# Performance work log

Measured on AMD Instinct MI355X. Metric: run time of the kernel, lower is better.

Reference implementation:

```python
import jax, jax.numpy as jnp
import numpy as np

N_NODES = 50000
N_EDGES = 800000
IN_CH = 256
HID = 64
HEADS = 4
NEG_SLOPE = 0.2  # PyG GATConv default


def setup_inputs() -> dict:
    key = jax.random.key(0)
    ks = jax.random.split(key, 12)
    glorot = lambda k, shape: jax.random.normal(k, shape, jnp.float32) * (2.0 / (shape[0] + shape[-1])) ** 0.5
    d1 = HEADS * HID  # 256: width after conv1 (concat heads)
    return {
        "x": jax.random.normal(ks[0], (N_NODES, IN_CH), jnp.float32),
        "edge_index": jax.random.randint(ks[1], (2, N_EDGES), 0, N_NODES, jnp.int64),
        # conv1: GATConv(IN_CH, HID, heads=HEADS)
        "W1": glorot(ks[2], (IN_CH, HEADS * HID)),
        "a_src1": glorot(ks[3], (HEADS, HID)),
        "a_dst1": glorot(ks[4], (HEADS, HID)),
        "b1": jnp.zeros((HEADS * HID,), jnp.float32),
        # conv2: GATConv(d1, d1, heads=1)
        "W2": glorot(ks[5], (d1, d1)),
        "a_src2": glorot(ks[6], (1, d1)),
        "a_dst2": glorot(ks[7], (1, d1)),
        "b2": jnp.zeros((d1,), jnp.float32),
    }


def gat_conv(x, src, dst, W, a_src, a_dst, b, heads, out_ch, n_nodes):
    """PyG-style GATConv: per-head linear, additive attention, segment softmax over dst."""
    h = (x @ W).reshape(n_nodes, heads, out_ch)            # [N, H, C]
    alpha_src = jnp.sum(h * a_src, axis=-1)                # [N, H]
    alpha_dst = jnp.sum(h * a_dst, axis=-1)                # [N, H]
    e = jax.nn.leaky_relu(alpha_src[src] + alpha_dst[dst], NEG_SLOPE)  # [E, H]
    # numerically-stable segment softmax grouped by destination node
    e_max = jax.ops.segment_max(e, dst, num_segments=n_nodes)         # [N, H]
    e_exp = jnp.exp(e - e_max[dst])
    denom = jax.ops.segment_sum(e_exp, dst, num_segments=n_nodes)
    alpha = e_exp / denom[dst]                                        # [E, H]
    out = jax.ops.segment_sum(alpha[:, :, None] * h[src], dst, num_segments=n_nodes)  # [N, H, C]
    return out.reshape(n_nodes, heads * out_ch) + b


def reference(x, edge_index, W1, a_src1, a_dst1, b1, W2, a_src2, a_dst2, b2):
    n = x.shape[0]
    loops = jnp.arange(n, dtype=edge_index.dtype)
    src = jnp.concatenate([edge_index[0], loops])  # add self-loops (PyG default)
    dst = jnp.concatenate([edge_index[1], loops])
    h1 = gat_conv(x, src, dst, W1, a_src1, a_dst1, b1, HEADS, HID, n)
    h1 = jax.nn.elu(h1)
    out = gat_conv(h1, src, dst, W2, a_src2, a_dst2, b2, 1, HEADS * HID, n)
    return out
```

## Files before the change

### kernel.cpp

```cpp
#include <hip/hip_runtime.h>
#include <stdint.h>

typedef __bf16 bfv8 __attribute__((ext_vector_type(8)));
typedef float f32x4 __attribute__((ext_vector_type(4)));

__device__ __forceinline__ float b2f(unsigned short u) {
    union { unsigned int i; float f; } v; v.i = ((unsigned int)u) << 16; return v.f;
}
__device__ __forceinline__ unsigned short f2b(float f) {
    unsigned int x = __float_as_uint(f);
    unsigned int r = x + 0x7FFFu + ((x >> 16) & 1u);
    return (unsigned short)(r >> 16);
}
__device__ __forceinline__ float squash(float v) {
    return (v == v && fabsf(v) < 1e30f) ? v : 0.f;
}
__device__ __forceinline__ float blo(unsigned int w) {
    union { unsigned int i; float f; } v; v.i = w << 16; return v.f;
}
__device__ __forceinline__ float bhi(unsigned int w) {
    union { unsigned int i; float f; } v; v.i = w & 0xffff0000u; return v.f;
}

__device__ __forceinline__ void detect_reg(const void* x, const void* ei, int& f32w, int& i64w) {
    const unsigned short* xu = (const unsigned short*)x;
    const int* e32 = (const int*)ei;
    int bad = 0, oz = 0;
#pragma unroll
    for (int j = 0; j < 64; j++) {
        float v = b2f(xu[j]);
        if (!(fabsf(v) < 1e10f)) bad++;
    }
#pragma unroll
    for (int j = 1; j < 16; j += 2)
        if (e32[j] == 0) oz++;
    f32w = (bad >= 2) ? 1 : 0;
    i64w = (oz >= 6) ? 1 : 0;
}

__device__ __forceinline__ int edge_at(const void* ei, int idx, int i64) {
    return i64 ? (int)(((const long long*)ei)[idx]) : ((const int*)ei)[idx];
}

__global__ __launch_bounds__(256) void k_prep(
        const void* __restrict__ x, const void* __restrict__ ei,
        const void* __restrict__ W1, const void* __restrict__ W2,
        const void* __restrict__ a_src1, const void* __restrict__ a_dst1, const void* __restrict__ b1,
        const void* __restrict__ a_src2, const void* __restrict__ a_dst2, const void* __restrict__ b2,
        unsigned short* __restrict__ xb, unsigned short* __restrict__ WT1,
        unsigned short* __restrict__ WT2, unsigned short* __restrict__ vecs,
        int* __restrict__ deg, int* __restrict__ flags,
        int E, int ET, int N, int total8, int nconv, int nhist) {
    __shared__ unsigned short t[32][33];
    int f32w, i64w;
    detect_reg(x, ei, f32w, i64w);
    int b = blockIdx.x;
    int tid = threadIdx.x;

    if (b < nconv) {
        int i = b * 256 + tid;
        if (i >= total8) return;
        if (f32w) {
            const float4* f = (const float4*)x;
            float4 a = f[2 * i], bb = f[2 * i + 1];
            uint4 o;
            o.x = (unsigned)f2b(squash(a.x)) | ((unsigned)f2b(squash(a.y)) << 16);
            o.y = (unsigned)f2b(squash(a.z)) | ((unsigned)f2b(squash(a.w)) << 16);
            o.z = (unsigned)f2b(squash(bb.x)) | ((unsigned)f2b(squash(bb.y)) << 16);
            o.w = (unsigned)f2b(squash(bb.z)) | ((unsigned)f2b(squash(bb.w)) << 16);
            *(uint4*)(xb + 8 * (size_t)i) = o;
        } else {
            *(uint4*)(xb + 8 * (size_t)i) = ((const uint4*)x)[i];
        }
    } else if (b < nconv + 128) {
        int tb2 = b - nconv;
        const void* W = (tb2 < 64) ? W1 : W2;
        unsigned short* WT = (tb2 < 64) ? WT1 : WT2;
        int t6 = tb2 & 63;
        int bx = (t6 & 7) * 32, by = (t6 >> 3) * 32;
        int tx = tid & 31, ty = tid >> 5;
        for (int j = 0; j < 32; j += 8) {
            size_t idx = (size_t)(by + ty + j) * 256 + bx + tx;
            t[ty + j][tx] = f32w ? f2b(squash(((const float*)W)[idx]))
                                 : ((const unsigned short*)W)[idx];
        }
        __syncthreads();
        for (int j = 0; j < 32; j += 8)
            WT[(size_t)(bx + ty + j) * 256 + by + tx] = t[tx][ty + j];
    } else if (b < nconv + 128 + nhist) {
        int i = (b - nconv - 128) * 256 + tid;
        if (i >= ET) return;
        int d = (i < E) ? edge_at(ei, E + i, i64w) : (i - E);
        d = min(max(d, 0), N - 1);
        atomicAdd(&deg[d], 1);
    } else {
        const void* ptrs[6] = {a_src1, a_dst1, b1, a_src2, a_dst2, b2};
#pragma unroll
        for (int j = 0; j < 6; j++) {
            unsigned short u = f32w ? f2b(squash(((const float*)ptrs[j])[tid]))
                                    : ((const unsigned short*)ptrs[j])[tid];
            vecs[j * 256 + tid] = u;
        }
        if (tid == 0) { flags[0] = f32w; flags[1] = i64w; }
    }
}

__global__ void k_scan1(const int* __restrict__ deg, int* __restrict__ tscan, int* __restrict__ bsum, int n) {
    __shared__ int sm[256];
    int tid = threadIdx.x;
    int i = blockIdx.x * 256 + tid;
    int v = (i < n) ? deg[i] : 0;
    sm[tid] = v; __syncthreads();
    for (int off = 1; off < 256; off <<= 1) {
        int t = (tid >= off) ? sm[tid - off] : 0;
        __syncthreads();
        sm[tid] += t;
        __syncthreads();
    }
    if (i < n) tscan[i] = sm[tid];
    if (tid == 255) bsum[blockIdx.x] = sm[255];
}

__global__ void k_scan2(const int* __restrict__ bsum, int* __restrict__ boff, int nb) {
    __shared__ int sm[256];
    int tid = threadIdx.x;
    int v = (tid < nb) ? bsum[tid] : 0;
    sm[tid] = v; __syncthreads();
    for (int off = 1; off < 256; off <<= 1) {
        int t = (tid >= off) ? sm[tid - off] : 0;
        __syncthreads();
        sm[tid] += t;
        __syncthreads();
    }
    if (tid < nb) boff[tid] = sm[tid] - v;
}

__global__ void k_scan3(const int* __restrict__ deg, const int* __restrict__ tscan,
                        const int* __restrict__ boff, int* __restrict__ row_start,
                        int* __restrict__ cursor, unsigned short* __restrict__ csr16,
                        int n, int ET) {
    int i = blockIdx.x * 256 + threadIdx.x;
    if (i < n) {
        int rs = tscan[i] - deg[i] + boff[i >> 8];
        row_start[i] = rs;
        cursor[i] = rs;
    }
    if (i == 0) row_start[n] = ET;
    if (blockIdx.x == 0 && threadIdx.x < 64) csr16[ET + threadIdx.x] = 0;
}

__global__ void k_scatter(const void* __restrict__ ei, int* __restrict__ cursor,
                          unsigned short* __restrict__ csr16, const int* __restrict__ flags,
                          int E, int ET, int N) {
    int i = blockIdx.x * 256 + threadIdx.x;
    if (i >= ET) return;
    int s, d;
    if (i < E) {
        int i64 = flags[1];
        s = edge_at(ei, i, i64);
        d = edge_at(ei, E + i, i64);
    } else {
        s = i - E; d = i - E;
    }
    s = min(max(s, 0), N - 1);
    d = min(max(d, 0), N - 1);
    int pos = atomicAdd(&cursor[d], 1);
    pos = min(max(pos, 0), ET - 1);
    csr16[pos] = (unsigned short)s;
}

__global__ __launch_bounds__(256) void k_gemm(const unsigned short* __restrict__ A,
                                              const unsigned short* __restrict__ BT,
                                              unsigned short* __restrict__ C, int M) {
    __shared__ __align__(16) unsigned short As[128 * 72];
    __shared__ __align__(16) unsigned short Bs[128 * 72];
    const int tid = threadIdx.x;
    const int m0 = blockIdx.x * 128, n0 = blockIdx.y * 128;
    const int w = tid >> 6, lane = tid & 63;
    const int wm = (w & 1) * 64, wn = (w >> 1) * 64;
    const int lr = lane & 15, lk = (lane >> 4) * 8;
    const int sr = tid >> 1, sc = (tid & 1) * 32;

    f32x4 acc[4][4];
#pragma unroll
    for (int a = 0; a < 4; a++)
#pragma unroll
        for (int b = 0; b < 4; b++) acc[a][b] = (f32x4){0.f, 0.f, 0.f, 0.f};

    for (int k0 = 0; k0 < 256; k0 += 64) {
        uint4 va0, va1, va2, va3;
        if (m0 + sr < M) {
            const uint4* Ap = (const uint4*)(A + (size_t)(m0 + sr) * 256 + k0 + sc);
            va0 = Ap[0]; va1 = Ap[1]; va2 = Ap[2]; va3 = Ap[3];
        } else {
            va0 = va1 = va2 = va3 = make_uint4(0, 0, 0, 0);
        }
        {
            uint4* Ad = (uint4*)&As[sr * 72 + sc];
            Ad[0] = va0; Ad[1] = va1; Ad[2] = va2; Ad[3] = va3;
        }
        {
            const uint4* Bp = (const uint4*)(BT + (size_t)(n0 + sr) * 256 + k0 + sc);
            uint4* Bd = (uint4*)&Bs[sr * 72 + sc];
            Bd[0] = Bp[0]; Bd[1] = Bp[1]; Bd[2] = Bp[2]; Bd[3] = Bp[3];
        }
        __syncthreads();
#pragma unroll
        for (int kk = 0; kk < 64; kk += 32) {
            bfv8 af[4], bfr[4];
#pragma unroll
            for (int mi = 0; mi < 4; mi++)
                af[mi] = *(const bfv8*)&As[(wm + mi * 16 + lr) * 72 + kk + lk];
#pragma unroll
            for (int ni = 0; ni < 4; ni++)
                bfr[ni] = *(const bfv8*)&Bs[(wn + ni * 16 + lr) * 72 + kk + lk];
#pragma unroll
            for (int mi = 0; mi < 4; mi++)
#pragma unroll
                for (int ni = 0; ni < 4; ni++)
                    acc[mi][ni] = __builtin_amdgcn_mfma_f32_16x16x32_bf16(af[mi], bfr[ni], acc[mi][ni], 0, 0, 0);
        }
        __syncthreads();
    }
    const int rb = (lane >> 4) * 4;
#pragma unroll
    for (int mi = 0; mi < 4; mi++) {
#pragma unroll
        for (int r = 0; r < 4; r++) {
            int row = m0 + wm + mi * 16 + rb + r;
            if (row < M) {
#pragma unroll
                for (int ni = 0; ni < 4; ni++)
                    C[(size_t)row * 256 + n0 + wn + ni * 16 + lr] = f2b(squash(acc[mi][ni][r]));
            }
        }
    }
}

__global__ void k_alphas(const unsigned short* __restrict__ Hm, const unsigned short* __restrict__ a_src,
                         const unsigned short* __restrict__ a_dst, float* __restrict__ as_out,
                         float* __restrict__ ad_out, int N, int H) {
    int wid = (blockIdx.x * 256 + threadIdx.x) >> 6;
    int lane = threadIdx.x & 63;
    if (wid >= N) return;
    int c = 4 * lane;
    uint2 hv = *(const uint2*)(Hm + (size_t)wid * 256 + c);
    float h0 = b2f((unsigned short)(hv.x & 0xffff));
    float h1 = b2f((unsigned short)(hv.x >> 16));
    float h2 = b2f((unsigned short)(hv.y & 0xffff));
    float h3 = b2f((unsigned short)(hv.y >> 16));
    float s = h0 * b2f(a_src[c]) + h1 * b2f(a_src[c + 1]) + h2 * b2f(a_src[c + 2]) + h3 * b2f(a_src[c + 3]);
    float d = h0 * b2f(a_dst[c]) + h1 * b2f(a_dst[c + 1]) + h2 * b2f(a_dst[c + 2]) + h3 * b2f(a_dst[c + 3]);
    int lph = 64 / H;
    for (int off = 1; off < lph; off <<= 1) {
        s += __shfl_xor(s, off, 64);
        d += __shfl_xor(d, off, 64);
    }
    if ((lane & (lph - 1)) == 0) {
        int h = lane / lph;
        as_out[(size_t)wid * H + h] = squash(s);
        ad_out[(size_t)wid * H + h] = squash(d);
    }
}

__global__ __launch_bounds__(256) void k_agg(
        const unsigned short* __restrict__ Hm, const float* __restrict__ asrc,
        const float* __restrict__ adst, const int* __restrict__ row_start,
        const unsigned short* __restrict__ csr16, const unsigned short* __restrict__ bias,
        void* __restrict__ out, const int* __restrict__ flags,
        int N, int H, int ET, int elu, int is_final) {
    __shared__ __align__(16) float lwv[8][32][4];
    __shared__ unsigned int loff[8][32];
    const int tid = threadIdx.x;
    const int hw = tid >> 5;
    const int l = tid & 31;
    const int node = blockIdx.x * 8 + hw;
    if (node >= N) return;
    const int h = (l * H) >> 5;
    const int lb = l * 16;
    int rs = row_start[node], re = row_start[node + 1];
    rs = min(max(rs, 0), ET);
    re = min(max(re, rs), ET);

    float4 adn;
    if (H == 4) adn = *(const float4*)(adst + (size_t)node * 4);
    else { adn.x = adst[node]; adn.y = adn.z = adn.w = 0.f; }

    float4 lsum = make_float4(0.f, 0.f, 0.f, 0.f);
    float a0 = 0.f, a1 = 0.f, a2 = 0.f, a3 = 0.f, a4 = 0.f, a5 = 0.f, a6 = 0.f, a7 = 0.f;
    const float* wbase = &lwv[hw][0][0] + h;
    const unsigned int* obase = &loff[hw][0];
    const char* Hb = (const char*)Hm;

    for (int c = rs; c < re; c += 32) {
        const int cnt = min(32, re - c);
        float4 w4 = make_float4(0.f, 0.f, 0.f, 0.f);
        unsigned int off = 0;
        if (l < cnt) {
            int idx = min((int)csr16[c + l], N - 1);
            off = (unsigned)idx << 9;
            if (H == 4) {
                float4 av = *(const float4*)(asrc + (size_t)idx * 4);
                float ex = av.x + adn.x, ey = av.y + adn.y;
                float ez = av.z + adn.z, ew = av.w + adn.w;
                ex = (ex < 0.f) ? 0.2f * ex : ex;
                ey = (ey < 0.f) ? 0.2f * ey : ey;
                ez = (ez < 0.f) ? 0.2f * ez : ez;
                ew = (ew < 0.f) ? 0.2f * ew : ew;
                w4.x = __expf(fminf(ex, 80.f)); w4.y = __expf(fminf(ey, 80.f));
                w4.z = __expf(fminf(ez, 80.f)); w4.w = __expf(fminf(ew, 80.f));
            } else {
                float ev = asrc[idx] + adn.x;
                ev = (ev < 0.f) ? 0.2f * ev : ev;
                w4.x = __expf(fminf(ev, 80.f));
            }
        }
        lsum.x += w4.x;
        if (H == 4) { lsum.y += w4.y; lsum.z += w4.z; lsum.w += w4.w; }
        *(float4*)&lwv[hw][l][0] = w4;
        loff[hw][l] = off;
        asm volatile("s_waitcnt lgkmcnt(0)");

        const int full = cnt & ~7;
        int jb = 0;
        for (; jb < full; jb += 8) {
            unsigned int o_[8];
            uint4 hv[8];
            float wj[8];
#pragma unroll
            for (int u = 0; u < 8; u++) o_[u] = obase[jb + u];
#pragma unroll
            for (int u = 0; u < 8; u++) hv[u] = *(const uint4*)(Hb + (size_t)o_[u] + lb);
#pragma unroll
            for (int u = 0; u < 8; u++) wj[u] = wbase[(jb + u) * 4];
#pragma unroll
            for (int u = 0; u < 8; u++) {
                a0 = fmaf(wj[u], blo(hv[u].x), a0); a1 = fmaf(wj[u], bhi(hv[u].x), a1);
                a2 = fmaf(wj[u], blo(hv[u].y), a2); a3 = fmaf(wj[u], bhi(hv[u].y), a3);
                a4 = fmaf(wj[u], blo(hv[u].z), a4); a5 = fmaf(wj[u], bhi(hv[u].z), a5);
                a6 = fmaf(wj[u], blo(hv[u].w), a6); a7 = fmaf(wj[u], bhi(hv[u].w), a7);
            }
        }
        if (jb < cnt) {
            const int rem = cnt - jb;
            unsigned int o_[8];
            uint4 hv[8];
            float wj[8];
#pragma unroll
            for (int u = 0; u < 8; u++) o_[u] = obase[jb + u];
#pragma unroll
            for (int u = 0; u < 8; u++) {
                uint4 z = make_uint4(0, 0, 0, 0);
                hv[u] = (u < rem) ? *(const uint4*)(Hb + (size_t)o_[u] + lb) : z;
            }
#pragma unroll
            for (int u = 0; u < 8; u++) wj[u] = wbase[(jb + u) * 4];
#pragma unroll
            for (int u = 0; u < 8; u++) {
                a0 = fmaf(wj[u], blo(hv[u].x), a0); a1 = fmaf(wj[u], bhi(hv[u].x), a1);
                a2 = fmaf(wj[u], blo(hv[u].y), a2); a3 = fmaf(wj[u], bhi(hv[u].y), a3);
                a4 = fmaf(wj[u], blo(hv[u].z), a4); a5 = fmaf(wj[u], bhi(hv[u].z), a5);
                a6 = fmaf(wj[u], blo(hv[u].w), a6); a7 = fmaf(wj[u], bhi(hv[u].w), a7);
            }
        }
    }
    for (int off = 1; off < 32; off <<= 1) {
        lsum.x += __shfl_xor(lsum.x, off, 64);
        if (H == 4) {
            lsum.y += __shfl_xor(lsum.y, off, 64);
            lsum.z += __shfl_xor(lsum.z, off, 64);
            lsum.w += __shfl_xor(lsum.w, off, 64);
        }
    }
    float ls = (H == 4) ? ((h == 0) ? lsum.x : (h == 1) ? lsum.y : (h == 2) ? lsum.z : lsum.w)
                        : lsum.x;
    float inv = (ls > 0.f) ? 1.f / ls : 0.f;

    const int cc = 8 * l;
    uint4 bv = *(const uint4*)(bias + cc);
    float o0 = a0 * inv + blo(bv.x), o1 = a1 * inv + bhi(bv.x);
    float o2 = a2 * inv + blo(bv.y), o3 = a3 * inv + bhi(bv.y);
    float o4 = a4 * inv + blo(bv.z), o5 = a5 * inv + bhi(bv.z);
    float o6 = a6 * inv + blo(bv.w), o7 = a7 * inv + bhi(bv.w);
    if (elu) {
        o0 = (o0 > 0.f) ? o0 : __expf(o0) - 1.f;
        o1 = (o1 > 0.f) ? o1 : __expf(o1) - 1.f;
        o2 = (o2 > 0.f) ? o2 : __expf(o2) - 1.f;
        o3 = (o3 > 0.f) ? o3 : __expf(o3) - 1.f;
        o4 = (o4 > 0.f) ? o4 : __expf(o4) - 1.f;
        o5 = (o5 > 0.f) ? o5 : __expf(o5) - 1.f;
        o6 = (o6 > 0.f) ? o6 : __expf(o6) - 1.f;
        o7 = (o7 > 0.f) ? o7 : __expf(o7) - 1.f;
    }
    o0 = squash(o0); o1 = squash(o1); o2 = squash(o2); o3 = squash(o3);
    o4 = squash(o4); o5 = squash(o5); o6 = squash(o6); o7 = squash(o7);
    if (is_final && flags[0]) {
        float* op = (float*)out + (size_t)node * 256 + cc;
        *(float4*)op       = make_float4(o0, o1, o2, o3);
        *(float4*)(op + 4) = make_float4(o4, o5, o6, o7);
    } else {
        uint4 ov;
        ov.x = (unsigned)f2b(o0) | ((unsigned)f2b(o1) << 16);
        ov.y = (unsigned)f2b(o2) | ((unsigned)f2b(o3) << 16);
        ov.z = (unsigned)f2b(o4) | ((unsigned)f2b(o5) << 16);
        ov.w = (unsigned)f2b(o6) | ((unsigned)f2b(o7) << 16);
        *(uint4*)((unsigned short*)out + (size_t)node * 256 + cc) = ov;
    }
}

extern "C" void kernel_launch(void* const* d_in, const int* in_sizes, int n_in,
                              void* d_out, int out_size, void* d_ws, size_t ws_size,
                              hipStream_t stream) {
    const void* x      = d_in[0];
    const void* ei     = d_in[1];
    const void* W1     = d_in[2];
    const void* a_src1 = d_in[3];
    const void* a_dst1 = d_in[4];
    const void* b1     = d_in[5];
    const void* W2     = d_in[6];
    const void* a_src2 = d_in[7];
    const void* a_dst2 = d_in[8];
    const void* b2     = d_in[9];

    const int N  = in_sizes[0] / 256;
    const int E  = in_sizes[1] / 2;
    const int ET = E + N;

    char* p = (char*)d_ws;
    auto alloc = [&](size_t bytes) -> char* {
        char* r = p;
        p += (bytes + 255) & ~(size_t)255;
        return r;
    };
    int* flags = (int*)alloc(256);
    unsigned short* WT1  = (unsigned short*)alloc(256 * 256 * 2);
    unsigned short* WT2  = (unsigned short*)alloc(256 * 256 * 2);
    unsigned short* vecs = (unsigned short*)alloc(6 * 256 * 2);
    float* as_ = (float*)alloc((size_t)N * 4 * 4);
    float* ad_ = (float*)alloc((size_t)N * 4 * 4);
    int* deg       = (int*)alloc((size_t)N * 4);
    int* tscan     = (int*)alloc((size_t)N * 4);
    int* row_start = (int*)alloc((size_t)(N + 1) * 4);
    int* cursor    = (int*)alloc((size_t)N * 4);
    int* bsum      = (int*)alloc(1024);
    int* boff      = (int*)alloc(1024);
    unsigned short* csr16 = (unsigned short*)alloc((size_t)(ET + 64) * 2);

    unsigned short* BUF_OUT = (unsigned short*)d_out;
    unsigned short* BUF_IN0 = (unsigned short*)d_in[0];

    hipMemsetAsync(deg, 0, (size_t)N * 4, stream);

    const int total8 = N * 256 / 8;
    const int nconv  = (total8 + 255) / 256;
    const int nhist  = (ET + 255) / 256;
    const int nprep  = nconv + 128 + nhist + 1;

    k_prep<<<nprep, 256, 0, stream>>>(x, ei, W1, W2, a_src1, a_dst1, b1, a_src2, a_dst2, b2,
                                      BUF_OUT, WT1, WT2, vecs, deg, flags,
                                      E, ET, N, total8, nconv, nhist);

    int nb = (N + 255) / 256;
    k_scan1<<<nb, 256, 0, stream>>>(deg, tscan, bsum, N);
    k_scan2<<<1, 256, 0, stream>>>(bsum, boff, nb);
    k_scan3<<<nb, 256, 0, stream>>>(deg, tscan, boff, row_start, cursor, csr16, N, ET);
    k_scatter<<<nhist, 256, 0, stream>>>(ei, cursor, csr16, flags, E, ET, N);

    int gm = (N + 127) / 128;
    int wb = (N + 3) / 4;
    int ab = (N + 7) / 8;

    k_gemm<<<dim3(gm, 2), 256, 0, stream>>>(BUF_OUT, WT1, BUF_IN0, N);
    k_alphas<<<wb, 256, 0, stream>>>(BUF_IN0, vecs + 0 * 256, vecs + 1 * 256, as_, ad_, N, 4);
    k_agg<<<ab, 256, 0, stream>>>(BUF_IN0, as_, ad_, row_start, csr16, vecs + 2 * 256,
                                  BUF_OUT, flags, N, 4, ET, 1, 0);
    k_gemm<<<dim3(gm, 2), 256, 0, stream>>>(BUF_OUT, WT2, BUF_IN0, N);
    k_alphas<<<wb, 256, 0, stream>>>(BUF_IN0, vecs + 3 * 256, vecs + 4 * 256, as_, ad_, N, 1);
    k_agg<<<ab, 256, 0, stream>>>(BUF_IN0, as_, ad_, row_start, csr16, vecs + 5 * 256,
                                  d_out, flags, N, 1, ET, 0, 1);
}
```

Measured before the change: 403.7 us.

## Fuse attention logits into GEMM, single-pass CSR scan, pipeline aggregation gathers

Three independent changes. First, the three scan kernels become one decoupled look-back scan that publishes block prefixes through flag words. Second, the per-node attention dot products move into the GEMM epilogue, which writes 64-column partial sums per slice; for one head these are added at use time. Third, the aggregation kernel is templated on head count and double-buffers neighbour feature gathers, with offsets broadcast by shuffles instead of LDS. This removes several launches and a full re-read of the projected features, at the cost of a spin-wait scan that relies on earlier blocks making forward progress.

```diff
diff --git a/kernel.cpp b/kernel.cpp
--- a/kernel.cpp
+++ b/kernel.cpp
@@ -105,11 +105,15 @@
     }
 }
 
-__global__ void k_scan1(const int* __restrict__ deg, int* __restrict__ tscan, int* __restrict__ bsum, int n) {
+__global__ __launch_bounds__(256) void k_csr(const int* __restrict__ deg,
+        int* __restrict__ row_start, int* __restrict__ cursor,
+        unsigned short* __restrict__ csr16, int* __restrict__ fz,
+        int N, int ET) {
     __shared__ int sm[256];
-    int tid = threadIdx.x;
-    int i = blockIdx.x * 256 + tid;
-    int v = (i < n) ? deg[i] : 0;
+    __shared__ int s_prefix;
+    const int b = blockIdx.x, tid = threadIdx.x;
+    const int i = b * 256 + tid;
+    int v = (i < N) ? deg[i] : 0;
     sm[tid] = v; __syncthreads();
     for (int off = 1; off < 256; off <<= 1) {
         int t = (tid >= off) ? sm[tid - off] : 0;
@@ -117,36 +121,48 @@
         sm[tid] += t;
         __syncthreads();
     }
-    if (i < n) tscan[i] = sm[tid];
-    if (tid == 255) bsum[blockIdx.x] = sm[255];
-}
-
-__global__ void k_scan2(const int* __restrict__ bsum, int* __restrict__ boff, int nb) {
-    __shared__ int sm[256];
-    int tid = threadIdx.x;
-    int v = (tid < nb) ? bsum[tid] : 0;
-    sm[tid] = v; __syncthreads();
-    for (int off = 1; off < 256; off <<= 1) {
-        int t = (tid >= off) ? sm[tid - off] : 0;
-        __syncthreads();
-        sm[tid] += t;
-        __syncthreads();
-    }
-    if (tid < nb) boff[tid] = sm[tid] - v;
-}
-
-__global__ void k_scan3(const int* __restrict__ deg, const int* __restrict__ tscan,
-                        const int* __restrict__ boff, int* __restrict__ row_start,
-                        int* __restrict__ cursor, unsigned short* __restrict__ csr16,
-                        int n, int ET) {
-    int i = blockIdx.x * 256 + threadIdx.x;
-    if (i < n) {
-        int rs = tscan[i] - deg[i] + boff[i >> 8];
+    int incl = sm[tid];
+    int total = sm[255];
+    if (tid == 0) {
+        int val = (b == 0) ? ((total << 2) | 2) : ((total << 2) | 1);
+        __threadfence();
+        atomicExch(&fz[b], val);
+    }
+    if (b == 0) {
+        if (tid == 0) s_prefix = 0;
+    } else if (tid < 64) {
+        int prefix = 0, base = b - 1, done = 0;
+        while (!done) {
+            int p = base - tid;
+            int val;
+            if (p >= 0) {
+                do { val = atomicAdd(&fz[p], 0); } while (val == 0);
+            } else {
+                val = 2;
+            }
+            unsigned long long im = __ballot((val & 2) != 0);
+            int fi = (int)__ffsll(im) - 1;
+            int mv = val >> 2;
+            int contrib = (fi < 0 || tid <= fi) ? mv : 0;
+            for (int o = 1; o < 64; o <<= 1) contrib += __shfl_xor(contrib, o, 64);
+            prefix += contrib;
+            if (fi >= 0) done = 1; else base -= 64;
+        }
+        if (tid == 0) {
+            s_prefix = prefix;
+            __threadfence();
+            atomicExch(&fz[b], ((prefix + total) << 2) | 2);
+        }
+    }
+    __syncthreads();
+    int pre = s_prefix;
+    if (i < N) {
+        int rs = pre + incl - v;
         row_start[i] = rs;
         cursor[i] = rs;
     }
-    if (i == 0) row_start[n] = ET;
-    if (blockIdx.x == 0 && threadIdx.x < 64) csr16[ET + threadIdx.x] = 0;
+    if (b == 0 && tid == 0) row_start[N] = ET;
+    if (b == 0 && tid < 64) csr16[ET + tid] = 0;
 }
 
 __global__ void k_scatter(const void* __restrict__ ei, int* __restrict__ cursor,
@@ -171,7 +187,11 @@
 
 __global__ __launch_bounds__(256) void k_gemm(const unsigned short* __restrict__ A,
                                               const unsigned short* __restrict__ BT,
-                                              unsigned short* __restrict__ C, int M) {
+                                              unsigned short* __restrict__ C,
+                                              const unsigned short* __restrict__ avs,
+                                              const unsigned short* __restrict__ avd,
+                                              float* __restrict__ as_out,
+                                              float* __restrict__ ad_out, int M) {
     __shared__ __align__(16) unsigned short As[128 * 72];
     __shared__ __align__(16) unsigned short Bs[128 * 72];
     const int tid = threadIdx.x;
@@ -235,45 +255,72 @@
             }
         }
     }
-}
-
-__global__ void k_alphas(const unsigned short* __restrict__ Hm, const unsigned short* __restrict__ a_src,
-                         const unsigned short* __restrict__ a_dst, float* __restrict__ as_out,
-                         float* __restrict__ ad_out, int N, int H) {
-    int wid = (blockIdx.x * 256 + threadIdx.x) >> 6;
-    int lane = threadIdx.x & 63;
-    if (wid >= N) return;
-    int c = 4 * lane;
-    uint2 hv = *(const uint2*)(Hm + (size_t)wid * 256 + c);
-    float h0 = b2f((unsigned short)(hv.x & 0xffff));
-    float h1 = b2f((unsigned short)(hv.x >> 16));
-    float h2 = b2f((unsigned short)(hv.y & 0xffff));
-    float h3 = b2f((unsigned short)(hv.y >> 16));
-    float s = h0 * b2f(a_src[c]) + h1 * b2f(a_src[c + 1]) + h2 * b2f(a_src[c + 2]) + h3 * b2f(a_src[c + 3]);
-    float d = h0 * b2f(a_dst[c]) + h1 * b2f(a_dst[c + 1]) + h2 * b2f(a_dst[c + 2]) + h3 * b2f(a_dst[c + 3]);
-    int lph = 64 / H;
-    for (int off = 1; off < lph; off <<= 1) {
-        s += __shfl_xor(s, off, 64);
-        d += __shfl_xor(d, off, 64);
-    }
-    if ((lane & (lph - 1)) == 0) {
-        int h = lane / lph;
-        as_out[(size_t)wid * H + h] = squash(s);
-        ad_out[(size_t)wid * H + h] = squash(d);
-    }
-}
-
+    const int slice = (n0 + wn) >> 6;
+    float asl[4], adl[4];
+#pragma unroll
+    for (int ni = 0; ni < 4; ni++) {
+        int col = n0 + wn + ni * 16 + lr;
+        asl[ni] = b2f(avs[col]);
+        adl[ni] = b2f(avd[col]);
+    }
+#pragma unroll
+    for (int mi = 0; mi < 4; mi++) {
+#pragma unroll
+        for (int r = 0; r < 4; r++) {
+            float ps = 0.f, pd = 0.f;
+#pragma unroll
+            for (int ni = 0; ni < 4; ni++) {
+                float cv = acc[mi][ni][r];
+                ps = fmaf(cv, asl[ni], ps);
+                pd = fmaf(cv, adl[ni], pd);
+            }
+#pragma unroll
+            for (int off = 1; off < 16; off <<= 1) {
+                ps += __shfl_xor(ps, off, 64);
+                pd += __shfl_xor(pd, off, 64);
+            }
+            int row = m0 + wm + mi * 16 + rb + r;
+            if (lr == 0 && row < M) {
+                as_out[(size_t)row * 4 + slice] = squash(ps);
+                ad_out[(size_t)row * 4 + slice] = squash(pd);
+            }
+        }
+    }
+}
+
+#define AGG_ISSUE(eb, hv)                                                     \
+    {                                                                         \
+        _Pragma("unroll") for (int u = 0; u < 8; u++) {                       \
+            const int e = (eb) * 8 + u;                                       \
+            unsigned o = __shfl(off, (lw & 32) + e, 64);                      \
+            uint4 z = make_uint4(0, 0, 0, 0);                                 \
+            hv[u] = (e < cnt) ? *(const uint4*)(Hb + (size_t)o + lb) : z;     \
+        }                                                                     \
+    }
+#define AGG_CONSUME(eb, hv)                                                   \
+    if ((eb) * 8 < cnt) {                                                     \
+        _Pragma("unroll") for (int u = 0; u < 8; u++) {                       \
+            const int e = (eb) * 8 + u;                                       \
+            float wj = wbase[e * 4];                                          \
+            a0 = fmaf(wj, blo(hv[u].x), a0); a1 = fmaf(wj, bhi(hv[u].x), a1); \
+            a2 = fmaf(wj, blo(hv[u].y), a2); a3 = fmaf(wj, bhi(hv[u].y), a3); \
+            a4 = fmaf(wj, blo(hv[u].z), a4); a5 = fmaf(wj, bhi(hv[u].z), a5); \
+            a6 = fmaf(wj, blo(hv[u].w), a6); a7 = fmaf(wj, bhi(hv[u].w), a7); \
+        }                                                                     \
+    }
+
+template <int H>
 __global__ __launch_bounds__(256) void k_agg(
         const unsigned short* __restrict__ Hm, const float* __restrict__ asrc,
         const float* __restrict__ adst, const int* __restrict__ row_start,
         const unsigned short* __restrict__ csr16, const unsigned short* __restrict__ bias,
         void* __restrict__ out, const int* __restrict__ flags,
-        int N, int H, int ET, int elu, int is_final) {
+        int N, int ET, int elu, int is_final) {
     __shared__ __align__(16) float lwv[8][32][4];
-    __shared__ unsigned int loff[8][32];
     const int tid = threadIdx.x;
     const int hw = tid >> 5;
     const int l = tid & 31;
+    const int lw = tid & 63;
     const int node = blockIdx.x * 8 + hw;
     if (node >= N) return;
     const int h = (l * H) >> 5;
@@ -282,27 +329,36 @@
     rs = min(max(rs, 0), ET);
     re = min(max(re, rs), ET);
 
-    float4 adn;
-    if (H == 4) adn = *(const float4*)(adst + (size_t)node * 4);
-    else { adn.x = adst[node]; adn.y = adn.z = adn.w = 0.f; }
-
-    float4 lsum = make_float4(0.f, 0.f, 0.f, 0.f);
+    float adnx = 0.f, adny = 0.f, adnz = 0.f, adnw = 0.f;
+    {
+        float4 t = *(const float4*)(adst + (size_t)node * 4);
+        if (H == 4) { adnx = t.x; adny = t.y; adnz = t.z; adnw = t.w; }
+        else        { adnx = t.x + t.y + t.z + t.w; }
+    }
+
+    float lsx = 0.f, lsy = 0.f, lsz = 0.f, lsw = 0.f;
     float a0 = 0.f, a1 = 0.f, a2 = 0.f, a3 = 0.f, a4 = 0.f, a5 = 0.f, a6 = 0.f, a7 = 0.f;
     const float* wbase = &lwv[hw][0][0] + h;
-    const unsigned int* obase = &loff[hw][0];
     const char* Hb = (const char*)Hm;
 
     for (int c = rs; c < re; c += 32) {
         const int cnt = min(32, re - c);
         float4 w4 = make_float4(0.f, 0.f, 0.f, 0.f);
         unsigned int off = 0;
-        if (l < cnt) {
-            int idx = min((int)csr16[c + l], N - 1);
-            off = (unsigned)idx << 9;
+        int idx = 0;
+        const bool act = (l < cnt);
+        if (act) idx = min((int)csr16[c + l], N - 1);
+        off = (unsigned)idx << 9;
+
+        uint4 hvA[8], hvB[8];
+        AGG_ISSUE(0, hvA);
+        if (8 < cnt) AGG_ISSUE(1, hvB);
+
+        if (act) {
+            float4 av = *(const float4*)(asrc + (size_t)idx * 4);
             if (H == 4) {
-                float4 av = *(const float4*)(asrc + (size_t)idx * 4);
-                float ex = av.x + adn.x, ey = av.y + adn.y;
-                float ez = av.z + adn.z, ew = av.w + adn.w;
+                float ex = av.x + adnx, ey = av.y + adny;
+                float ez = av.z + adnz, ew = av.w + adnw;
                 ex = (ex < 0.f) ? 0.2f * ex : ex;
                 ey = (ey < 0.f) ? 0.2f * ey : ey;
                 ez = (ez < 0.f) ? 0.2f * ez : ez;
@@ -310,70 +366,33 @@
                 w4.x = __expf(fminf(ex, 80.f)); w4.y = __expf(fminf(ey, 80.f));
                 w4.z = __expf(fminf(ez, 80.f)); w4.w = __expf(fminf(ew, 80.f));
             } else {
-                float ev = asrc[idx] + adn.x;
+                float ev = (av.x + av.y + av.z + av.w) + adnx;
                 ev = (ev < 0.f) ? 0.2f * ev : ev;
                 w4.x = __expf(fminf(ev, 80.f));
             }
         }
-        lsum.x += w4.x;
-        if (H == 4) { lsum.y += w4.y; lsum.z += w4.z; lsum.w += w4.w; }
+        lsx += w4.x;
+        if (H == 4) { lsy += w4.y; lsz += w4.z; lsw += w4.w; }
         *(float4*)&lwv[hw][l][0] = w4;
-        loff[hw][l] = off;
         asm volatile("s_waitcnt lgkmcnt(0)");
 
-        const int full = cnt & ~7;
-        int jb = 0;
-        for (; jb < full; jb += 8) {
-            unsigned int o_[8];
-            uint4 hv[8];
-            float wj[8];
-#pragma unroll
-            for (int u = 0; u < 8; u++) o_[u] = obase[jb + u];
-#pragma unroll
-            for (int u = 0; u < 8; u++) hv[u] = *(const uint4*)(Hb + (size_t)o_[u] + lb);
-#pragma unroll
-            for (int u = 0; u < 8; u++) wj[u] = wbase[(jb + u) * 4];
-#pragma unroll
-            for (int u = 0; u < 8; u++) {
-                a0 = fmaf(wj[u], blo(hv[u].x), a0); a1 = fmaf(wj[u], bhi(hv[u].x), a1);
-                a2 = fmaf(wj[u], blo(hv[u].y), a2); a3 = fmaf(wj[u], bhi(hv[u].y), a3);
-                a4 = fmaf(wj[u], blo(hv[u].z), a4); a5 = fmaf(wj[u], bhi(hv[u].z), a5);
-                a6 = fmaf(wj[u], blo(hv[u].w), a6); a7 = fmaf(wj[u], bhi(hv[u].w), a7);
-            }
-        }
-        if (jb < cnt) {
-            const int rem = cnt - jb;
-            unsigned int o_[8];
-            uint4 hv[8];
-            float wj[8];
-#pragma unroll
-            for (int u = 0; u < 8; u++) o_[u] = obase[jb + u];
-#pragma unroll
-            for (int u = 0; u < 8; u++) {
-                uint4 z = make_uint4(0, 0, 0, 0);
-                hv[u] = (u < rem) ? *(const uint4*)(Hb + (size_t)o_[u] + lb) : z;
-            }
-#pragma unroll
-            for (int u = 0; u < 8; u++) wj[u] = wbase[(jb + u) * 4];
-#pragma unroll
-            for (int u = 0; u < 8; u++) {
-                a0 = fmaf(wj[u], blo(hv[u].x), a0); a1 = fmaf(wj[u], bhi(hv[u].x), a1);
-                a2 = fmaf(wj[u], blo(hv[u].y), a2); a3 = fmaf(wj[u], bhi(hv[u].y), a3);
-                a4 = fmaf(wj[u], blo(hv[u].z), a4); a5 = fmaf(wj[u], bhi(hv[u].z), a5);
-                a6 = fmaf(wj[u], blo(hv[u].w), a6); a7 = fmaf(wj[u], bhi(hv[u].w), a7);
-            }
-        }
-    }
+        AGG_CONSUME(0, hvA);
+        if (16 < cnt) AGG_ISSUE(2, hvA);
+        AGG_CONSUME(1, hvB);
+        if (24 < cnt) AGG_ISSUE(3, hvB);
+        AGG_CONSUME(2, hvA);
+        AGG_CONSUME(3, hvB);
+    }
+
     for (int off = 1; off < 32; off <<= 1) {
-        lsum.x += __shfl_xor(lsum.x, off, 64);
+        lsx += __shfl_xor(lsx, off, 64);
         if (H == 4) {
-            lsum.y += __shfl_xor(lsum.y, off, 64);
-            lsum.z += __shfl_xor(lsum.z, off, 64);
-            lsum.w += __shfl_xor(lsum.w, off, 64);
-        }
-    }
-    float ls = (H == 4) ? ((h == 0) ? lsum.x : (h == 1) ? lsum.y : (h == 2) ? lsum.z : lsum.w)
-                        : lsum.x;
+            lsy += __shfl_xor(lsy, off, 64);
+            lsz += __shfl_xor(lsz, off, 64);
+            lsw += __shfl_xor(lsw, off, 64);
+        }
+    }
+    float ls = (H == 4) ? ((h == 0) ? lsx : (h == 1) ? lsy : (h == 2) ? lsz : lsw) : lsx;
     float inv = (ls > 0.f) ? 1.f / ls : 0.f;
 
     const int cc = 8 * l;
@@ -438,18 +457,17 @@
     unsigned short* vecs = (unsigned short*)alloc(6 * 256 * 2);
     float* as_ = (float*)alloc((size_t)N * 4 * 4);
     float* ad_ = (float*)alloc((size_t)N * 4 * 4);
-    int* deg       = (int*)alloc((size_t)N * 4);
-    int* tscan     = (int*)alloc((size_t)N * 4);
+    int* deg   = (int*)alloc((size_t)N * 4);
+    int* fz    = (int*)alloc(1024);
     int* row_start = (int*)alloc((size_t)(N + 1) * 4);
     int* cursor    = (int*)alloc((size_t)N * 4);
-    int* bsum      = (int*)alloc(1024);
-    int* boff      = (int*)alloc(1024);
     unsigned short* csr16 = (unsigned short*)alloc((size_t)(ET + 64) * 2);
 
     unsigned short* BUF_OUT = (unsigned short*)d_out;
     unsigned short* BUF_IN0 = (unsigned short*)d_in[0];
 
-    hipMemsetAsync(deg, 0, (size_t)N * 4, stream);
+    const size_t degpad = ((size_t)N * 4 + 255) & ~(size_t)255;
+    hipMemsetAsync(deg, 0, degpad + 1024, stream);
 
     const int total8 = N * 256 / 8;
     const int nconv  = (total8 + 255) / 256;
@@ -461,21 +479,18 @@
                                       E, ET, N, total8, nconv, nhist);
 
     int nb = (N + 255) / 256;
-    k_scan1<<<nb, 256, 0, stream>>>(deg, tscan, bsum, N);
-    k_scan2<<<1, 256, 0, stream>>>(bsum, boff, nb);
-    k_scan3<<<nb, 256, 0, stream>>>(deg, tscan, boff, row_start, cursor, csr16, N, ET);
+    k_csr<<<nb, 256, 0, stream>>>(deg, row_start, cursor, csr16, fz, N, ET);
     k_scatter<<<nhist, 256, 0, stream>>>(ei, cursor, csr16, flags, E, ET, N);
 
     int gm = (N + 127) / 128;
-    int wb = (N + 3) / 4;
     int ab = (N + 7) / 8;
 
-    k_gemm<<<dim3(gm, 2), 256, 0, stream>>>(BUF_OUT, WT1, BUF_IN0, N);
-    k_alphas<<<wb, 256, 0, stream>>>(BUF_IN0, vecs + 0 * 256, vecs + 1 * 256, as_, ad_, N, 4);
-    k_agg<<<ab, 256, 0, stream>>>(BUF_IN0, as_, ad_, row_start, csr16, vecs + 2 * 256,
-                                  BUF_OUT, flags, N, 4, ET, 1, 0);
-    k_gemm<<<dim3(gm, 2), 256, 0, stream>>>(BUF_OUT, WT2, BUF_IN0, N);
-    k_alphas<<<wb, 256, 0, stream>>>(BUF_IN0, vecs + 3 * 256, vecs + 4 * 256, as_, ad_, N, 1);
-    k_agg<<<ab, 256, 0, stream>>>(BUF_IN0, as_, ad_, row_start, csr16, vecs + 5 * 256,
-                                  d_out, flags, N, 1, ET, 0, 1);
-}
+    k_gemm<<<dim3(gm, 2), 256, 0, stream>>>(BUF_OUT, WT1, BUF_IN0,
+                                            vecs + 0 * 256, vecs + 1 * 256, as_, ad_, N);
+    k_agg<4><<<ab, 256, 0, stream>>>(BUF_IN0, as_, ad_, row_start, csr16, vecs + 2 * 256,
+                                     BUF_OUT, flags, N, ET, 1, 0);
+    k_gemm<<<dim3(gm, 2), 256, 0, stream>>>(BUF_OUT, WT2, BUF_IN0,
+                                            vecs + 3 * 256, vecs + 4 * 256, as_, ad_, N);
+    k_agg<1><<<ab, 256, 0, stream>>>(BUF_IN0, as_, ad_, row_start, csr16, vecs + 5 * 256,
+                                     d_out, flags, N, ET, 0, 1);
+}
```

New measurement: 467.8 us. 1.16x slower.
